# Kernel tuning notes

Hardware: AMD Instinct MI355X
Metric: run time of the kernel (lower is better)

The kernel has to match this reference:

```python
import jax, jax.numpy as jnp
import numpy as np

DIM = 256
N_TAPES = 4
HEAD_DIM = 64  # mem_size
HT = HEAD_DIM * N_TAPES  # 256
QKVA = 3 * HT + 11 * N_TAPES  # 812
EPS = 1e-12


def _normalize(x, axis):
    n = jnp.sqrt(jnp.sum(x * x, axis=axis, keepdims=True))
    return x / jnp.maximum(n, EPS)


def setup_inputs() -> dict:
    key = jax.random.key(0)
    ks = jax.random.split(key, 8)
    L_tgt, L_src, B = 128, 64, 512
    s = 1.0 / np.sqrt(DIM)
    return {
        "tgt": jax.random.normal(ks[0], (L_tgt, B, DIM), jnp.float32),
        "src": jax.random.normal(ks[1], (L_src, B, DIM), jnp.float32),
        "W_ih": jax.random.uniform(ks[2], (4 * DIM, DIM), jnp.float32, -s, s),
        "W_hh": jax.random.uniform(ks[3], (4 * DIM, DIM), jnp.float32, -s, s),
        "b_ih": jax.random.uniform(ks[4], (4 * DIM,), jnp.float32, -s, s),
        "b_hh": jax.random.uniform(ks[5], (4 * DIM,), jnp.float32, -s, s),
        "Wqkva_w": jax.random.uniform(ks[6], (QKVA, DIM), jnp.float32, -s, s),
        "Wqkva_b": jax.random.uniform(ks[7], (QKVA,), jnp.float32, -s, s),
    }


def _step(carry, x, W_ih, W_hh, b_ih, b_hh, Wqkva_w, Wqkva_b):
    tape, rpos, wpos, h, c = carry  # tape: [L,B,T,C], rpos/wpos: [L,B,T]
    B = x.shape[0]
    # LSTMCell (torch gate order: i, f, g, o)
    gates = x @ W_ih.T + b_ih + h @ W_hh.T + b_hh
    i, f, g, o = jnp.split(gates, 4, axis=-1)
    c = jax.nn.sigmoid(f) * c + jax.nn.sigmoid(i) * jnp.tanh(g)
    h = jax.nn.sigmoid(o) * jnp.tanh(c)
    qkva = h @ Wqkva_w.T + Wqkva_b  # [B, 812]
    query = _normalize(qkva[:, :HT].reshape(B, N_TAPES, HEAD_DIM), axis=-1)
    # note: `key` slice in the original is empty and unused
    value = qkva[:, 2 * HT:3 * HT].reshape(B, N_TAPES, HEAD_DIM)
    action = qkva[:, 3 * HT:].reshape(B, N_TAPES, 11)
    read_dir = jax.nn.softmax(action[:, :, :4], axis=-1)
    write_dir = jax.nn.softmax(action[:, :, 4:8], axis=-1)
    rwe = jax.nn.sigmoid(action[:, :, 8:])
    oldval = jnp.einsum('lbtc,lbt->btc', tape, wpos)
    newmem = jnp.einsum('lbt,btc->lbtc', wpos,
                        value * rwe[:, :, 1:2] - oldval * rwe[:, :, 2:3])
    ntape = tape + newmem
    rval = jnp.einsum('lbtc,lbt->btc', tape, rpos * rwe[:, :, 0]).reshape(B, -1)
    jpos = _normalize(jnp.einsum('lbtc,btc->lbt', tape, query), axis=0)
    next_w = jnp.roll(wpos, 1, axis=0)
    prev_w = jnp.roll(wpos, -1, axis=0)
    nwpos = (prev_w * write_dir[None, :, :, 0] + wpos * write_dir[None, :, :, 1]
             + next_w * write_dir[None, :, :, 2] + jpos * write_dir[None, :, :, 3])
    next_r = jnp.roll(rpos, 1, axis=0)
    prev_r = jnp.roll(rpos, -1, axis=0)
    nrpos = (prev_r * read_dir[None, :, :, 0] + rpos * read_dir[None, :, :, 1]
             + next_r * read_dir[None, :, :, 2] + jpos * read_dir[None, :, :, 3])
    return (ntape, nrpos, nwpos, h, c), rval


def reference(tgt, src, W_ih, W_hh, b_ih, b_hh, Wqkva_w, Wqkva_b):
    L_src, B = src.shape[0], src.shape[1]
    tape = src.reshape(L_src, B, N_TAPES, HEAD_DIM)
    pos0 = jnp.zeros((L_src, B, N_TAPES), src.dtype).at[0].set(1.0)
    h = jnp.zeros((B, DIM), src.dtype)
    c = jnp.zeros((B, DIM), src.dtype)

    def step(carry, x):
        return _step(carry, x, W_ih, W_hh, b_ih, b_hh, Wqkva_w, Wqkva_b)

    _, read_outs = jax.lax.scan(step, (tape, pos0, pos0, h, c), tgt)
    return read_outs  # [seqlen, B, dim]
```

## Files before the change

### kernel.cpp

```cpp
#include <hip/hip_runtime.h>
#include <hip/hip_bf16.h>

typedef short short8_v __attribute__((ext_vector_type(8)));
typedef float f32x4 __attribute__((ext_vector_type(4)));

#define QC 576

__device__ __forceinline__ size_t swz_e(int r, int k, int KC) {
  return ((size_t)((r >> 4) * KC + (k >> 5)) * 64 + (r & 15) + (((k >> 3) & 3) << 4)) * 8 + (k & 7);
}

__device__ __forceinline__ float wave_sum(float v) {
#pragma unroll
  for (int off = 32; off > 0; off >>= 1) v += __shfl_xor(v, off);
  return v;
}

__device__ __forceinline__ float sigf(float x) { return 1.f / (1.f + __expf(-x)); }
__device__ __forceinline__ float tfast(float x) {
  float e = __expf(2.f * x);
  return 1.f - 2.f / (e + 1.f);
}

template <typename T>
__device__ __forceinline__ T ald(const T* p) {
  return __hip_atomic_load(p, __ATOMIC_RELAXED, __HIP_MEMORY_SCOPE_AGENT);
}
template <typename T>
__device__ __forceinline__ void ast(T* p, T v) {
  __hip_atomic_store(p, v, __ATOMIC_RELAXED, __HIP_MEMORY_SCOPE_AGENT);
}


__global__ void prep_weights(const float* __restrict__ W_ih, const float* __restrict__ W_hh,
                             __hip_bfloat16* __restrict__ Wcat) {
  int idx = blockIdx.x * blockDim.x + threadIdx.x;
  if (idx >= 1024 * 512) return;
  int jj = idx >> 9, k = idx & 511;
  int chunk = jj >> 6, gate = (jj >> 4) & 3, r = jj & 15;
  int j = gate * 256 + chunk * 16 + r;
  float v = (k < 256) ? W_ih[j * 256 + k] : W_hh[j * 256 + (k - 256)];
  Wcat[swz_e(jj, k, 16)] = __float2bfloat16(v);
}

__global__ void prep_wq(const float* __restrict__ Wq_w, const float* __restrict__ Wq_b,
                        __hip_bfloat16* __restrict__ Wq, float* __restrict__ biasq) {
  int idx = blockIdx.x * blockDim.x + threadIdx.x;
  if (idx >= 576 * 256) return;
  int n = idx >> 8, k = idx & 255;
  int orig = (n < 256) ? n : (n < 556 ? n + 256 : -1);
  float v = (orig >= 0) ? Wq_w[orig * 256 + k] : 0.f;
  Wq[swz_e(n, k, 8)] = __float2bfloat16(v);
  if (k == 0) biasq[n] = (orig >= 0) ? Wq_b[orig] : 0.f;
}

__global__ void prep_tgt(const float* __restrict__ tgt, __hip_bfloat16* __restrict__ tswz) {
  for (size_t idx = (size_t)blockIdx.x * blockDim.x + threadIdx.x; idx < (size_t)128 * 131072;
       idx += (size_t)gridDim.x * blockDim.x) {
    int t = (int)(idx >> 17);
    int rem = (int)(idx & 131071);
    int b = rem >> 8, k = rem & 255;
    tswz[(size_t)t * 131072 + swz_e(b, k, 8)] = __float2bfloat16(tgt[idx]);
  }
}

__global__ void reset_bars(unsigned* __restrict__ bars) {
  int i = blockIdx.x * blockDim.x + threadIdx.x;
  if (i < 2048) bars[i] = 0u;
}

#define DYN_LDS 159744

__global__ __launch_bounds__(512, 2) void persist(
    const short8_v* __restrict__ tswz, const short8_v* __restrict__ Wcat,
    const short8_v* __restrict__ Wq, const float* __restrict__ biasq,
    const float* __restrict__ b_ih, const float* __restrict__ b_hh,
    unsigned short* __restrict__ hG,
    float* __restrict__ qkva,
    float* __restrict__ out, const float* __restrict__ src, unsigned* __restrict__ bars) {
  extern __shared__ float lds[];
  const int tid = threadIdx.x;
  const int w = tid >> 6, lane = tid & 63;
  const int m = blockIdx.x & 31, cgrp = blockIdx.x >> 5;
  unsigned* grpbar = bars + m * 64;

  f32x4* Tc = (f32x4*)lds + (size_t)w * 1024;
  float* S = lds + 32768 + w * 384;
  float* gbuf = lds + 35840;
  unsigned long long* hstage_u64 = (unsigned long long*)(lds + 37888);
  const short8_v* hstage_s8 = (const short8_v*)(lds + 37888);

  const int g = lane >> 4, c4 = lane & 15;

  const int b = 16 * m + 2 * cgrp + (w >> 2);
  const int tp = w & 3;
#pragma unroll
  for (int i = 0; i < 16; ++i) {
    int row = i * 4 + g;
    f32x4 v = *(const f32x4*)(src + (size_t)row * 131072 + b * 256 + tp * 64 + c4 * 4);
    Tc[row * 16 + (c4 ^ (row & 15))] = v;
  }
#pragma unroll
  for (int k = 0; k < 6; ++k) S[k * 64 + lane] = 0.f;
  float rp = (lane == 0) ? 1.f : 0.f, wp = rp;

  const int erow = tid >> 5, ecol = tid & 31;
  const int jh = 32 * cgrp + ecol;
  const float bI = b_ih[jh] + b_hh[jh];
  const float bF = b_ih[256 + jh] + b_hh[256 + jh];
  const float bG_ = b_ih[512 + jh] + b_hh[512 + jh];
  const float bO = b_ih[768 + jh] + b_hh[768 + jh];
  float c_reg = 0.f;
  const unsigned hIdx32 =
      (unsigned)(((m * 8 + cgrp) * 64 + erow + 16 * (ecol >> 3)) * 4 + ((ecol >> 1) & 3));

  const int qcnt = (cgrp < 4) ? 5 : 4;
  const int qst = (cgrp < 4) ? cgrp * 5 : 20 + (cgrp - 4) * 4;
  const int qtile = qst + w;

  short8_v bFr[16];
#pragma unroll
  for (int kc = 0; kc < 16; ++kc) bFr[kc] = Wcat[((cgrp * 8 + w) * 16 + kc) * 64 + lane];
  short8_v bQ[8];
  float bqv = 0.f;
  int n0 = 0;
  if (w < qcnt) {
    n0 = qtile * 16 + (lane & 15);
    bqv = biasq[n0];
#pragma unroll
    for (int kc = 0; kc < 8; ++kc) bQ[kc] = Wq[(qtile * 8 + kc) * 64 + lane];
  }

#pragma unroll 1
  for (int p = 0; p <= 129; ++p) {
    const int hrd = (p + 1) & 1, hwr = p & 1;
    const int s = p - 2;
    const int par = s & 1;

    float a_[11];
    f32x4 q4, val4;
    if (s >= 0) {
      const float* qrow = qkva + (size_t)(s & 1) * (512 * QC) + (size_t)b * QC;
#pragma unroll
      for (int j = 0; j < 11; ++j) a_[j] = ald(qrow + 512 + tp * 11 + j);
      unsigned long long u0 = ald((const unsigned long long*)(qrow + tp * 64 + c4 * 4));
      unsigned long long u1 = ald((const unsigned long long*)(qrow + tp * 64 + c4 * 4 + 2));
      unsigned long long v0 = ald((const unsigned long long*)(qrow + 256 + tp * 64 + c4 * 4));
      unsigned long long v1 = ald((const unsigned long long*)(qrow + 256 + tp * 64 + c4 * 4 + 2));
      float2 qa = __builtin_bit_cast(float2, u0), qb = __builtin_bit_cast(float2, u1);
      float2 va = __builtin_bit_cast(float2, v0), vb = __builtin_bit_cast(float2, v1);
      q4 = (f32x4){qa.x, qa.y, qb.x, qb.y};
      val4 = (f32x4){va.x, va.y, vb.x, vb.y};
    }
    short8_v aF[8];
    if (p < 128) {
      const short8_v* xg = tswz + (size_t)p * 16384;
#pragma unroll
      for (int kc = 0; kc < 8; ++kc) aF[kc] = xg[(m * 8 + kc) * 64 + lane];
    }
    if (p >= 1 && p <= 128) {
      const unsigned long long* hsrc = (const unsigned long long*)(hG + (size_t)hrd * 131072) +
                                       ((size_t)(m * 8 + w) * 64 + lane) * 2;
      unsigned long long lo = ald(hsrc), hi = ald(hsrc + 1);
      hstage_u64[((size_t)w * 64 + lane) * 2] = lo;
      hstage_u64[((size_t)w * 64 + lane) * 2 + 1] = hi;
    }
    __syncthreads();
    if (p < 128) {
      f32x4 acc = {0.f, 0.f, 0.f, 0.f};
#pragma unroll
      for (int kc = 0; kc < 8; ++kc)
        acc = __builtin_amdgcn_mfma_f32_16x16x32_bf16(aF[kc], bFr[kc], acc, 0, 0, 0);
      if (p > 0) {
#pragma unroll
        for (int kc = 8; kc < 16; ++kc) {
          short8_v a = hstage_s8[(kc - 8) * 64 + lane];
          acc = __builtin_amdgcn_mfma_f32_16x16x32_bf16(a, bFr[kc], acc, 0, 0, 0);
        }
      }
      int cl = w >> 2, gate = w & 3;
#pragma unroll
      for (int r = 0; r < 4; ++r)
        gbuf[((cl * 4 + gate) * 16 + ((lane >> 4) * 4 + r)) * 16 + (lane & 15)] = acc[r];
    }
    __syncthreads();
    if (p < 128) {
      float gi = gbuf[(((ecol >> 4) * 4 + 0) * 16 + erow) * 16 + (ecol & 15)] + bI;
      float gf = gbuf[(((ecol >> 4) * 4 + 1) * 16 + erow) * 16 + (ecol & 15)] + bF;
      float gg = gbuf[(((ecol >> 4) * 4 + 2) * 16 + erow) * 16 + (ecol & 15)] + bG_;
      float go = gbuf[(((ecol >> 4) * 4 + 3) * 16 + erow) * 16 + (ecol & 15)] + bO;
      float cc = sigf(gf) * c_reg + sigf(gi) * tfast(gg);
      c_reg = cc;
      float hh = sigf(go) * tfast(cc);
      __hip_bfloat16 hb16 = __float2bfloat16(hh);
      unsigned own = (unsigned)(*(unsigned short*)&hb16);
      unsigned other = (unsigned)__shfl_xor((int)own, 1) & 0xFFFFu;
      if ((ecol & 1) == 0) {
        unsigned pack = (other << 16) | own;
        ast((unsigned*)(hG + (size_t)hwr * 131072) + hIdx32, pack);
      }
    }
    if (p >= 1 && p <= 128 && w < qcnt) {
      f32x4 qa = {0.f, 0.f, 0.f, 0.f};
#pragma unroll
      for (int kc = 0; kc < 8; ++kc)
        qa = __builtin_amdgcn_mfma_f32_16x16x32_bf16(hstage_s8[kc * 64 + lane], bQ[kc], qa, 0, 0, 0);
      float* qw = qkva + (size_t)((p - 1) & 1) * (512 * QC);
#pragma unroll
      for (int r = 0; r < 4; ++r)
        ast(&qw[(size_t)(16 * m + (lane >> 4) * 4 + r) * QC + n0], qa[r] + bqv);
    }
    asm volatile("s_waitcnt vmcnt(0)" ::: "memory");
    __syncthreads();
    if (tid == 0 && p < 129)
      __hip_atomic_fetch_add(grpbar, 1u, __ATOMIC_RELAXED, __HIP_MEMORY_SCOPE_AGENT);
    if (s >= 0) {
      float m1 = fmaxf(fmaxf(a_[0], a_[1]), fmaxf(a_[2], a_[3]));
      float e0 = __expf(a_[0] - m1), e1 = __expf(a_[1] - m1), e2 = __expf(a_[2] - m1),
            e3 = __expf(a_[3] - m1);
      float inv = 1.f / (e0 + e1 + e2 + e3);
      float rd0 = e0 * inv, rd1 = e1 * inv, rd2 = e2 * inv, rd3 = e3 * inv;
      float m2 = fmaxf(fmaxf(a_[4], a_[5]), fmaxf(a_[6], a_[7]));
      float f0 = __expf(a_[4] - m2), f1 = __expf(a_[5] - m2), f2 = __expf(a_[6] - m2),
            f3 = __expf(a_[7] - m2);
      float inv2 = 1.f / (f0 + f1 + f2 + f3);
      float wd0 = f0 * inv2, wd1 = f1 * inv2, wd2 = f2 * inv2, wd3 = f3 * inv2;
      float rwe0 = sigf(a_[8]), rwe1 = sigf(a_[9]), rwe2 = sigf(a_[10]);
      float ss = q4[0] * q4[0] + q4[1] * q4[1] + q4[2] * q4[2] + q4[3] * q4[3];
#pragma unroll
      for (int off = 1; off < 16; off <<= 1) ss += __shfl_xor(ss, off);
      float qninv = 1.f / fmaxf(sqrtf(ss), 1e-12f);
      f32x4 qn4 = q4 * qninv;
      *(float2*)&S[par * 128 + lane * 2] = make_float2(wp, rp * rwe0);
      if (g == 0) *(f32x4*)&S[256 + c4 * 4] = qn4;
      f32x4 dv4 = *(const f32x4*)&S[320 + c4 * 4];
      f32x4 oa = {0.f, 0.f, 0.f, 0.f}, ra = oa;
#pragma unroll
      for (int i = 0; i < 16; ++i) {
        int row = i * 4 + g;
        float2 wrO = *(const float2*)&S[(par ^ 1) * 128 + row * 2];
        float2 wrN = *(const float2*)&S[par * 128 + row * 2];
        int ti = row * 16 + (c4 ^ (row & 15));
        f32x4 v = Tc[ti];
        v += wrO.x * dv4;
        Tc[ti] = v;
        oa += wrN.x * v;
        ra += wrN.y * v;
      }
#pragma unroll
      for (int off = 16; off <= 32; off <<= 1) {
        f32x4 t;
        t[0] = __shfl_xor(oa[0], off); t[1] = __shfl_xor(oa[1], off);
        t[2] = __shfl_xor(oa[2], off); t[3] = __shfl_xor(oa[3], off);
        oa += t;
        t[0] = __shfl_xor(ra[0], off); t[1] = __shfl_xor(ra[1], off);
        t[2] = __shfl_xor(ra[2], off); t[3] = __shfl_xor(ra[3], off);
        ra += t;
      }
      f32x4 dvn = val4 * rwe1 - oa * rwe2;
      if (g == 0) {
        *(f32x4*)&S[320 + c4 * 4] = dvn;
        *(f32x4*)(out + (size_t)s * 131072 + b * 256 + tp * 64 + c4 * 4) = ra;
      }
      float jq = 0.f;
#pragma unroll
      for (int j = 0; j < 16; ++j) {
        f32x4 v = Tc[lane * 16 + (j ^ (lane & 15))];
        f32x4 qv = *(const f32x4*)&S[256 + j * 4];
        jq += v[0] * qv[0] + v[1] * qv[1] + v[2] * qv[2] + v[3] * qv[3];
      }
      float jsum = wave_sum(jq * jq);
      float jp = jq / fmaxf(sqrtf(jsum), 1e-12f);
      float next_w = __shfl(wp, (lane + 63) & 63);
      float prev_w = __shfl(wp, (lane + 1) & 63);
      float next_r = __shfl(rp, (lane + 63) & 63);
      float prev_r = __shfl(rp, (lane + 1) & 63);
      wp = prev_w * wd0 + wp * wd1 + next_w * wd2 + jp * wd3;
      rp = prev_r * rd0 + rp * rd1 + next_r * rd2 + jp * rd3;
    }
    if (p < 129) {
      __syncthreads();
      if (tid == 0) {
        unsigned target = 8u * (unsigned)(p + 1);
        while (ald(grpbar) < target) __builtin_amdgcn_s_sleep(2);
        asm volatile("" ::: "memory");
      }
      __syncthreads();
    }
  }
}


extern "C" void kernel_launch(void* const* d_in, const int* in_sizes, int n_in, void* d_out,
                              int out_size, void* d_ws, size_t ws_size, hipStream_t stream) {
  const float* tgt = (const float*)d_in[0];
  const float* src = (const float*)d_in[1];
  const float* W_ih = (const float*)d_in[2];
  const float* W_hh = (const float*)d_in[3];
  const float* b_ih = (const float*)d_in[4];
  const float* b_hh = (const float*)d_in[5];
  const float* Wq_w = (const float*)d_in[6];
  const float* Wq_b = (const float*)d_in[7];
  float* out = (float*)d_out;

  char* ws = (char*)d_ws;
  size_t off = 0;
  auto alloc = [&](size_t bytes) -> void* {
    void* p = ws + off;
    off = (off + bytes + 255) & ~(size_t)255;
    return p;
  };
  unsigned* bars = (unsigned*)alloc(2048 * 4);
  float* qkva = (float*)alloc((size_t)2 * 512 * QC * 4);
  unsigned short* hG = (unsigned short*)alloc((size_t)2 * 131072 * 2);
  __hip_bfloat16* Wcat = (__hip_bfloat16*)alloc((size_t)1024 * 512 * 2);
  __hip_bfloat16* Wq = (__hip_bfloat16*)alloc((size_t)576 * 256 * 2);
  float* biasq = (float*)alloc((size_t)576 * 4);
  __hip_bfloat16* tswz = (__hip_bfloat16*)alloc((size_t)128 * 131072 * 2);

  reset_bars<<<8, 256, 0, stream>>>(bars);
  prep_weights<<<2048, 256, 0, stream>>>(W_ih, W_hh, Wcat);
  prep_wq<<<576, 256, 0, stream>>>(Wq_w, Wq_b, Wq, biasq);
  prep_tgt<<<8192, 256, 0, stream>>>(tgt, tswz);

  hipFuncSetAttribute((const void*)persist, hipFuncAttributeMaxDynamicSharedMemorySize, DYN_LDS);

  const short8_v* tswz_p = (const short8_v*)tswz;
  const short8_v* Wcat_p = (const short8_v*)Wcat;
  const short8_v* Wq_p = (const short8_v*)Wq;
  const float* biasq_p = biasq;
  const float* bih_p = b_ih;
  const float* bhh_p = b_hh;
  unsigned short* hG_p = hG;
  float* qkva_p = qkva;
  float* out_p = out;
  const float* src_p = src;
  unsigned* bars_p = bars;
  void* kargs[] = {(void*)&tswz_p, (void*)&Wcat_p, (void*)&Wq_p,  (void*)&biasq_p,
                   (void*)&bih_p,  (void*)&bhh_p,  (void*)&hG_p,  (void*)&qkva_p,
                   (void*)&out_p,  (void*)&src_p,  (void*)&bars_p};
  hipLaunchCooperativeKernel((const void*)persist, dim3(256), dim3(512), kargs,
                             (unsigned)DYN_LDS, stream);
}
```

Before: 959.3 us.

## Split persistent kernel into 512 blocks of 4 waves, one batch row each

The persistent cooperative kernel goes from 256 blocks of 512 threads to 512 blocks of 256 threads. Each block now owns one batch row (four tapes) and 16 hidden columns, so each group barrier counts 16 arrivals instead of 8. The previous-step write weights and delta vector now stay in registers (read through shuffles) instead of double-buffered LDS, and the launch switches from cooperative to a plain launch with a timeout on the spin barrier. The aim is finer-grained parallelism and less LDS traffic and footprint. The cost is more blocks per group barrier, and co-residency of all blocks is no longer guaranteed, which the timeout only partly covers.

```diff
diff --git a/kernel.cpp b/kernel.cpp
--- a/kernel.cpp
+++ b/kernel.cpp
@@ -69,9 +69,9 @@
   if (i < 2048) bars[i] = 0u;
 }
 
-#define DYN_LDS 159744
-
-__global__ __launch_bounds__(512, 2) void persist(
+#define DYN_LDS 79872
+
+__global__ __launch_bounds__(256, 2) void persist(
     const short8_v* __restrict__ tswz, const short8_v* __restrict__ Wcat,
     const short8_v* __restrict__ Wq, const float* __restrict__ biasq,
     const float* __restrict__ b_ih, const float* __restrict__ b_hh,
@@ -85,42 +85,44 @@
   unsigned* grpbar = bars + m * 64;
 
   f32x4* Tc = (f32x4*)lds + (size_t)w * 1024;
-  float* S = lds + 32768 + w * 384;
-  float* gbuf = lds + 35840;
-  unsigned long long* hstage_u64 = (unsigned long long*)(lds + 37888);
-  const short8_v* hstage_s8 = (const short8_v*)(lds + 37888);
+  float* WS = lds + 16384 + w * 128;
+  float* gbuf = lds + 16896;
+  float* QN = lds + 16896 + w * 64;
+  unsigned long long* hstage_u64 = (unsigned long long*)(lds + 17920);
+  const short8_v* hstage_s8 = (const short8_v*)(lds + 17920);
 
   const int g = lane >> 4, c4 = lane & 15;
 
-  const int b = 16 * m + 2 * cgrp + (w >> 2);
-  const int tp = w & 3;
+  const int b = 16 * m + cgrp;
+  const int tp = w;
 #pragma unroll
   for (int i = 0; i < 16; ++i) {
     int row = i * 4 + g;
     f32x4 v = *(const f32x4*)(src + (size_t)row * 131072 + b * 256 + tp * 64 + c4 * 4);
     Tc[row * 16 + (c4 ^ (row & 15))] = v;
   }
-#pragma unroll
-  for (int k = 0; k < 6; ++k) S[k * 64 + lane] = 0.f;
   float rp = (lane == 0) ? 1.f : 0.f, wp = rp;
-
-  const int erow = tid >> 5, ecol = tid & 31;
-  const int jh = 32 * cgrp + ecol;
+  float wpPrev = 0.f;
+  f32x4 dvp4 = {0.f, 0.f, 0.f, 0.f};
+  bool bar_ok = true;
+
+  const int erow = tid >> 4, ecol = tid & 15;
+  const int jh = 16 * cgrp + ecol;
   const float bI = b_ih[jh] + b_hh[jh];
   const float bF = b_ih[256 + jh] + b_hh[256 + jh];
   const float bG_ = b_ih[512 + jh] + b_hh[512 + jh];
   const float bO = b_ih[768 + jh] + b_hh[768 + jh];
   float c_reg = 0.f;
   const unsigned hIdx32 =
-      (unsigned)(((m * 8 + cgrp) * 64 + erow + 16 * (ecol >> 3)) * 4 + ((ecol >> 1) & 3));
-
-  const int qcnt = (cgrp < 4) ? 5 : 4;
-  const int qst = (cgrp < 4) ? cgrp * 5 : 20 + (cgrp - 4) * 4;
+      (unsigned)(((m * 8 + (jh >> 5)) * 64 + erow + 16 * ((jh >> 3) & 3)) * 4 + ((jh >> 1) & 3));
+
+  const int qcnt = (cgrp < 4) ? 3 : 2;
+  const int qst = (cgrp < 4) ? 3 * cgrp : 12 + 2 * (cgrp - 4);
   const int qtile = qst + w;
 
   short8_v bFr[16];
 #pragma unroll
-  for (int kc = 0; kc < 16; ++kc) bFr[kc] = Wcat[((cgrp * 8 + w) * 16 + kc) * 64 + lane];
+  for (int kc = 0; kc < 16; ++kc) bFr[kc] = Wcat[((4 * cgrp + w) * 16 + kc) * 64 + lane];
   short8_v bQ[8];
   float bqv = 0.f;
   int n0 = 0;
@@ -135,7 +137,6 @@
   for (int p = 0; p <= 129; ++p) {
     const int hrd = (p + 1) & 1, hwr = p & 1;
     const int s = p - 2;
-    const int par = s & 1;
 
     float a_[11];
     f32x4 q4, val4;
@@ -159,11 +160,13 @@
       for (int kc = 0; kc < 8; ++kc) aF[kc] = xg[(m * 8 + kc) * 64 + lane];
     }
     if (p >= 1 && p <= 128) {
-      const unsigned long long* hsrc = (const unsigned long long*)(hG + (size_t)hrd * 131072) +
-                                       ((size_t)(m * 8 + w) * 64 + lane) * 2;
-      unsigned long long lo = ald(hsrc), hi = ald(hsrc + 1);
-      hstage_u64[((size_t)w * 64 + lane) * 2] = lo;
-      hstage_u64[((size_t)w * 64 + lane) * 2 + 1] = hi;
+      const unsigned long long* hsrc =
+          (const unsigned long long*)(hG + (size_t)hrd * 131072) + (size_t)m * 1024;
+#pragma unroll
+      for (int j = 0; j < 4; ++j) {
+        unsigned long long v = ald(hsrc + tid + 256 * j);
+        hstage_u64[tid + 256 * j] = v;
+      }
     }
     __syncthreads();
     if (p < 128) {
@@ -178,17 +181,16 @@
           acc = __builtin_amdgcn_mfma_f32_16x16x32_bf16(a, bFr[kc], acc, 0, 0, 0);
         }
       }
-      int cl = w >> 2, gate = w & 3;
 #pragma unroll
       for (int r = 0; r < 4; ++r)
-        gbuf[((cl * 4 + gate) * 16 + ((lane >> 4) * 4 + r)) * 16 + (lane & 15)] = acc[r];
+        gbuf[(w * 16 + ((lane >> 4) * 4 + r)) * 16 + (lane & 15)] = acc[r];
     }
     __syncthreads();
     if (p < 128) {
-      float gi = gbuf[(((ecol >> 4) * 4 + 0) * 16 + erow) * 16 + (ecol & 15)] + bI;
-      float gf = gbuf[(((ecol >> 4) * 4 + 1) * 16 + erow) * 16 + (ecol & 15)] + bF;
-      float gg = gbuf[(((ecol >> 4) * 4 + 2) * 16 + erow) * 16 + (ecol & 15)] + bG_;
-      float go = gbuf[(((ecol >> 4) * 4 + 3) * 16 + erow) * 16 + (ecol & 15)] + bO;
+      float gi = gbuf[(0 * 16 + erow) * 16 + ecol] + bI;
+      float gf = gbuf[(1 * 16 + erow) * 16 + ecol] + bF;
+      float gg = gbuf[(2 * 16 + erow) * 16 + ecol] + bG_;
+      float go = gbuf[(3 * 16 + erow) * 16 + ecol] + bO;
       float cc = sigf(gf) * c_reg + sigf(gi) * tfast(gg);
       c_reg = cc;
       float hh = sigf(go) * tfast(cc);
@@ -231,18 +233,17 @@
       for (int off = 1; off < 16; off <<= 1) ss += __shfl_xor(ss, off);
       float qninv = 1.f / fmaxf(sqrtf(ss), 1e-12f);
       f32x4 qn4 = q4 * qninv;
-      *(float2*)&S[par * 128 + lane * 2] = make_float2(wp, rp * rwe0);
-      if (g == 0) *(f32x4*)&S[256 + c4 * 4] = qn4;
-      f32x4 dv4 = *(const f32x4*)&S[320 + c4 * 4];
+      *(float2*)&WS[lane * 2] = make_float2(wp, rp * rwe0);
+      if (g == 0) *(f32x4*)&QN[c4 * 4] = qn4;
       f32x4 oa = {0.f, 0.f, 0.f, 0.f}, ra = oa;
 #pragma unroll
       for (int i = 0; i < 16; ++i) {
         int row = i * 4 + g;
-        float2 wrO = *(const float2*)&S[(par ^ 1) * 128 + row * 2];
-        float2 wrN = *(const float2*)&S[par * 128 + row * 2];
+        float wO = __shfl(wpPrev, row);
+        float2 wrN = *(const float2*)&WS[row * 2];
         int ti = row * 16 + (c4 ^ (row & 15));
         f32x4 v = Tc[ti];
-        v += wrO.x * dv4;
+        v += wO * dvp4;
         Tc[ti] = v;
         oa += wrN.x * v;
         ra += wrN.y * v;
@@ -257,16 +258,14 @@
         t[2] = __shfl_xor(ra[2], off); t[3] = __shfl_xor(ra[3], off);
         ra += t;
       }
-      f32x4 dvn = val4 * rwe1 - oa * rwe2;
-      if (g == 0) {
-        *(f32x4*)&S[320 + c4 * 4] = dvn;
+      dvp4 = val4 * rwe1 - oa * rwe2;
+      if (g == 0)
         *(f32x4*)(out + (size_t)s * 131072 + b * 256 + tp * 64 + c4 * 4) = ra;
-      }
       float jq = 0.f;
 #pragma unroll
       for (int j = 0; j < 16; ++j) {
         f32x4 v = Tc[lane * 16 + (j ^ (lane & 15))];
-        f32x4 qv = *(const f32x4*)&S[256 + j * 4];
+        f32x4 qv = *(const f32x4*)&QN[j * 4];
         jq += v[0] * qv[0] + v[1] * qv[1] + v[2] * qv[2] + v[3] * qv[3];
       }
       float jsum = wave_sum(jq * jq);
@@ -275,14 +274,24 @@
       float prev_w = __shfl(wp, (lane + 1) & 63);
       float next_r = __shfl(rp, (lane + 63) & 63);
       float prev_r = __shfl(rp, (lane + 1) & 63);
+      wpPrev = wp;
       wp = prev_w * wd0 + wp * wd1 + next_w * wd2 + jp * wd3;
       rp = prev_r * rd0 + rp * rd1 + next_r * rd2 + jp * rd3;
     }
     if (p < 129) {
       __syncthreads();
       if (tid == 0) {
-        unsigned target = 8u * (unsigned)(p + 1);
-        while (ald(grpbar) < target) __builtin_amdgcn_s_sleep(2);
+        unsigned target = 16u * (unsigned)(p + 1);
+        if (bar_ok) {
+          long long t0 = (long long)__builtin_amdgcn_s_memrealtime();
+          while (ald(grpbar) < target) {
+            __builtin_amdgcn_s_sleep(8);
+            if ((long long)__builtin_amdgcn_s_memrealtime() - t0 > 100000000LL) {
+              bar_ok = false;
+              break;
+            }
+          }
+        }
         asm volatile("" ::: "memory");
       }
       __syncthreads();
@@ -325,20 +334,7 @@
 
   hipFuncSetAttribute((const void*)persist, hipFuncAttributeMaxDynamicSharedMemorySize, DYN_LDS);
 
-  const short8_v* tswz_p = (const short8_v*)tswz;
-  const short8_v* Wcat_p = (const short8_v*)Wcat;
-  const short8_v* Wq_p = (const short8_v*)Wq;
-  const float* biasq_p = biasq;
-  const float* bih_p = b_ih;
-  const float* bhh_p = b_hh;
-  unsigned short* hG_p = hG;
-  float* qkva_p = qkva;
-  float* out_p = out;
-  const float* src_p = src;
-  unsigned* bars_p = bars;
-  void* kargs[] = {(void*)&tswz_p, (void*)&Wcat_p, (void*)&Wq_p,  (void*)&biasq_p,
-                   (void*)&bih_p,  (void*)&bhh_p,  (void*)&hG_p,  (void*)&qkva_p,
-                   (void*)&out_p,  (void*)&src_p,  (void*)&bars_p};
-  hipLaunchCooperativeKernel((const void*)persist, dim3(256), dim3(512), kargs,
-                             (unsigned)DYN_LDS, stream);
-}
+  persist<<<dim3(512), dim3(256), DYN_LDS, stream>>>(
+      (const short8_v*)tswz, (const short8_v*)Wcat, (const short8_v*)Wq, biasq, b_ih, b_hh, hG,
+      qkva, out, src, bars);
+}
```

Result: slower. 1.002 ms (+4.4%).
